# Kernel tuning notes

Hardware: AMD Instinct MI355X
Metric: run time of the kernel (lower is better)

The kernel has to match this reference:

```python
import jax, jax.numpy as jnp
import numpy as np

N = 100000
D = 128
E = 1600000
NEG_SLOPE = 0.2


def gatv2_layer(x, src, dst, Wl, Wr, att, b):
    # GATv2Conv (heads=1, eval mode): lin_l -> source/message feats, lin_r -> target feats
    xl = x @ Wl                      # [N, D]
    xr = x @ Wr                      # [N, D]
    # per-edge score: a^T LeakyReLU(x_l[src] + x_r[dst])
    z = jax.nn.leaky_relu(xl[src] + xr[dst], NEG_SLOPE)  # [E, D]
    e = z @ att                      # [E]
    # segment softmax over incoming edges of each dst node
    m = jax.ops.segment_max(e, dst, num_segments=N)      # [N]
    ex = jnp.exp(e - m[dst])
    s = jax.ops.segment_sum(ex, dst, num_segments=N)     # [N]
    alpha = ex / (s[dst] + 1e-16)                        # [E]
    # weighted scatter-aggregate of source messages
    out = jax.ops.segment_sum(alpha[:, None] * xl[src], dst, num_segments=N)
    return out + b


def setup_inputs() -> dict:
    key = jax.random.key(0)
    ks = jax.random.split(key, 6)
    scale = 1.0 / np.sqrt(D)
    x = jax.random.normal(ks[0], (N, D), dtype=jnp.float32)
    edge_index = jax.random.randint(ks[1], (2, E), 0, N, dtype=jnp.int64)
    Wl = jax.random.normal(ks[2], (3, D, D), dtype=jnp.float32) * scale
    Wr = jax.random.normal(ks[3], (3, D, D), dtype=jnp.float32) * scale
    att = jax.random.normal(ks[4], (3, D), dtype=jnp.float32) * scale
    b = jax.random.normal(ks[5], (3, D), dtype=jnp.float32) * 0.01
    return {"x": x, "Wl": Wl, "Wr": Wr, "att": att, "b": b, "edge_index": edge_index}


def reference(x, Wl, Wr, att, b, edge_index):
    src, dst = edge_index[0], edge_index[1]
    h = gatv2_layer(x, src, dst, Wl[0], Wr[0], att[0], b[0])
    h = jax.nn.relu(h)
    h = gatv2_layer(h, src, dst, Wl[1], Wr[1], att[1], b[1])
    h = jax.nn.relu(h)
    h = gatv2_layer(h, src, dst, Wl[2], Wr[2], att[2], b[2])
    return h
```

## Files before the change

### kernel.cpp

```cpp
#include <hip/hip_runtime.h>
#include <math.h>

#define DD 128
#define NEG 0.2f

typedef short short8 __attribute__((ext_vector_type(8)));
typedef float f32x4 __attribute__((ext_vector_type(4)));
typedef float f32x2 __attribute__((ext_vector_type(2)));
typedef _Float16 h2v __attribute__((ext_vector_type(2)));

__device__ __forceinline__ unsigned short f2bf(float f) {
    unsigned u = __float_as_uint(f);
    return (unsigned short)((u + 0x7fffu + ((u >> 16) & 1u)) >> 16);
}
__device__ __forceinline__ float bf2f(unsigned short h) {
    return __uint_as_float(((unsigned)h) << 16);
}

#if __has_builtin(__builtin_amdgcn_exp2f)
#define EXP2F(x) __builtin_amdgcn_exp2f(x)
#else
#define EXP2F(x) exp2f(x)
#endif

__device__ void excl_scan_1024(int* sh, int* aux) {
    __syncthreads();
    int t = threadIdx.x;
    int base = t * 4;
    int a0 = sh[base], a1 = sh[base + 1], a2 = sh[base + 2], a3 = sh[base + 3];
    int s = a0 + a1 + a2 + a3;
    aux[t] = s;
    __syncthreads();
    for (int off = 1; off < 256; off <<= 1) {
        int v = (t >= off) ? aux[t - off] : 0;
        __syncthreads();
        aux[t] += v;
        __syncthreads();
    }
    int excl = aux[t] - s;
    sh[base] = excl;
    sh[base + 1] = excl + a0;
    sh[base + 2] = excl + a0 + a1;
    sh[base + 3] = excl + a0 + a1 + a2;
    __syncthreads();
}

__global__ __launch_bounds__(256) void k_histC(const int* __restrict__ dst,
                                               int* __restrict__ histC, int E, int CB,
                                               const float* __restrict__ Wl,
                                               const float* __restrict__ Wr,
                                               unsigned short* __restrict__ Wth,
                                               unsigned short* __restrict__ Wtl) {
    __shared__ int h[1024];
    int t = threadIdx.x;
    if (blockIdx.x >= 256) {
        int idx = (blockIdx.x - 256) * 256 + t;
        if (idx < 3 * 256 * 128) {
            int L = idx >> 15;
            int rem = idx & 32767;
            int nn = rem >> 7;
            int k = rem & 127;
            float v = (nn < 128) ? Wl[L * 16384 + k * 128 + nn]
                                 : Wr[L * 16384 + k * 128 + (nn - 128)];
            unsigned short hh = f2bf(v);
            Wth[idx] = hh;
            Wtl[idx] = f2bf(v - bf2f(hh));
        }
        return;
    }
    for (int j = t; j < 1024; j += 256) h[j] = 0;
    __syncthreads();
    int stride = 256 * 256;
    for (int i = blockIdx.x * 256 + t; i < E; i += stride)
        atomicAdd(&h[dst[i] >> 7], 1);
    __syncthreads();
    for (int j = t; j < CB; j += 256)
        if (h[j]) atomicAdd(&histC[j], h[j]);
}

#define CHUNK 8192
__global__ __launch_bounds__(256) void k_part3(const int* __restrict__ srcI,
                                               const int* __restrict__ dstI,
                                               const int* __restrict__ histC,
                                               int* __restrict__ cursor0C,
                                               int* __restrict__ baseC,
                                               uint2* __restrict__ part,
                                               int E, int CB) {
    __shared__ int sh[1024];
    __shared__ int gsh[1024];
    __shared__ int aux[256];
    __shared__ int resBase[1024];
    __shared__ int cur[1024];
    __shared__ uint2 stage[CHUNK];
    int t = threadIdx.x;
    int c0 = blockIdx.x * CHUNK;
    int cnt = E - c0; if (cnt > CHUNK) cnt = CHUNK;

    for (int j = t; j < 1024; j += 256) sh[j] = 0;
    for (int j = t; j < 1024; j += 256) gsh[j] = (j < CB) ? histC[j] : 0;
    __syncthreads();
    for (int i = t; i < cnt; i += 256)
        atomicAdd(&sh[dstI[c0 + i] >> 7], 1);
    excl_scan_1024(gsh, aux);
    for (int j = t; j < CB; j += 256) {
        int c = sh[j];
        resBase[j] = gsh[j] + (c ? atomicAdd(&cursor0C[j], c) : 0);
    }
    if (blockIdx.x == 0)
        for (int j = t; j <= CB; j += 256) baseC[j] = gsh[j];
    excl_scan_1024(sh, aux);
    for (int j = t; j < 1024; j += 256) cur[j] = sh[j];
    __syncthreads();
    for (int i = t; i < cnt; i += 256) {
        unsigned s = (unsigned)srcI[c0 + i];
        unsigned d = (unsigned)dstI[c0 + i];
        int b = (int)(d >> 7);
        int pos = atomicAdd(&cur[b], 1);
        stage[pos].x = s;
        stage[pos].y = d;
    }
    __syncthreads();
    for (int i = t; i < cnt; i += 256) {
        uint2 v = stage[i];
        int b = (int)(v.y >> 7);
        part[resBase[b] + (i - sh[b])] = v;
    }
}

__global__ __launch_bounds__(256) void k_part4(const uint2* __restrict__ part,
                                               const int* __restrict__ baseC,
                                               int* __restrict__ srcs,
                                               int* __restrict__ row_ptr,
                                               int N) {
    __shared__ int hist[128];
    __shared__ int incl[128];
    __shared__ int cur[128];
    __shared__ unsigned srcS[8192];
    int b = blockIdx.x;
    int t = threadIdx.x;
    int base = baseC[b];
    int cnt = baseC[b + 1] - base;
    int node0 = b << 7;

    if (t < 128) hist[t] = 0;
    __syncthreads();
    for (int i = t; i < cnt; i += 256)
        atomicAdd(&hist[part[base + i].y & 127], 1);
    __syncthreads();
    if (t < 128) incl[t] = hist[t];
    __syncthreads();
    for (int off = 1; off < 128; off <<= 1) {
        int v = 0;
        if (t < 128 && t >= off) v = incl[t - off];
        __syncthreads();
        if (t < 128) incl[t] += v;
        __syncthreads();
    }
    if (t < 128) cur[t] = incl[t] - hist[t];
    __syncthreads();
    for (int i = t; i < cnt; i += 256) {
        uint2 e = part[base + i];
        int r = atomicAdd(&cur[e.y & 127], 1);
        if (r < 8192) srcS[r] = e.x;
    }
    __syncthreads();
    for (int i = t; i < cnt; i += 256)
        srcs[base + i] = (int)srcS[i];
    int nodes = N - node0; if (nodes > 128) nodes = 128;
    if (t < nodes) row_ptr[node0 + t + 1] = base + incl[t];
    if (b == 0 && t == 0) row_ptr[0] = 0;
}

#define NCH 8192
__global__ __launch_bounds__(256) void k_deghist(const int* __restrict__ row_ptr,
                                                 int* __restrict__ histD, int N) {
    __shared__ int h[128];
    int t = threadIdx.x;
    if (t < 128) h[t] = 0;
    __syncthreads();
    int c0 = blockIdx.x * NCH;
    int cnt = N - c0; if (cnt > NCH) cnt = NCH;
    for (int i = t; i < cnt; i += 256) {
        int deg = row_ptr[c0 + i + 1] - row_ptr[c0 + i];
        int c = deg < 127 ? deg : 127;
        atomicAdd(&h[c], 1);
    }
    __syncthreads();
    if (t < 128 && h[t]) atomicAdd(&histD[t], h[t]);
}

__global__ __launch_bounds__(256) void k_degpart(const int* __restrict__ row_ptr,
                                                 const int* __restrict__ histD,
                                                 int* __restrict__ cursor0D,
                                                 int* __restrict__ order, int N) {
    __shared__ int hist[128];
    __shared__ int gex[128];
    __shared__ int excl[128];
    __shared__ int cur[128];
    __shared__ int resB[128];
    __shared__ int stage[NCH];
    int t = threadIdx.x;
    int c0 = blockIdx.x * NCH;
    int cnt = N - c0; if (cnt > NCH) cnt = NCH;

    int g0 = 0;
    if (t < 128) { hist[t] = 0; g0 = histD[t]; gex[t] = g0; }
    __syncthreads();
    for (int i = t; i < cnt; i += 256) {
        int deg = row_ptr[c0 + i + 1] - row_ptr[c0 + i];
        int c = deg < 127 ? deg : 127;
        atomicAdd(&hist[c], 1);
    }
    __syncthreads();
    for (int off = 1; off < 128; off <<= 1) {
        int v = 0;
        if (t < 128 && t >= off) v = gex[t - off];
        __syncthreads();
        if (t < 128) gex[t] += v;
        __syncthreads();
    }
    if (t < 128) resB[t] = (gex[t] - g0) + (hist[t] ? atomicAdd(&cursor0D[t], hist[t]) : 0);
    if (t < 128) excl[t] = hist[t];
    __syncthreads();
    for (int off = 1; off < 128; off <<= 1) {
        int v = 0;
        if (t < 128 && t >= off) v = excl[t - off];
        __syncthreads();
        if (t < 128) excl[t] += v;
        __syncthreads();
    }
    if (t < 128) { excl[t] -= hist[t]; cur[t] = excl[t]; }
    __syncthreads();
    for (int i = t; i < cnt; i += 256) {
        int deg = row_ptr[c0 + i + 1] - row_ptr[c0 + i];
        int c = deg < 127 ? deg : 127;
        int p = atomicAdd(&cur[c], 1);
        stage[p] = (c << 20) | (c0 + i);
    }
    __syncthreads();
    for (int i = t; i < cnt; i += 256) {
        int v = stage[i];
        int c = v >> 20;
        order[resB[c] + (i - excl[c])] = v & 0xFFFFF;
    }
}

__device__ __forceinline__ void cvt8(const float4& a, const float4& b, uint4& hi, uint4& lo) {
    union US8 { unsigned short s[8]; uint4 u; } H, Lo;
    float f[8] = {a.x, a.y, a.z, a.w, b.x, b.y, b.z, b.w};
#pragma unroll
    for (int i = 0; i < 8; i++) {
        unsigned short h = f2bf(f[i]);
        H.s[i] = h;
        Lo.s[i] = f2bf(f[i] - bf2f(h));
    }
    hi = H.u; lo = Lo.u;
}

template <int F32SRC>
__global__ __launch_bounds__(256) void k_gemm(const float* __restrict__ Xf,
                                              const unsigned short* __restrict__ Ahi,
                                              const unsigned short* __restrict__ Alo,
                                              const unsigned short* __restrict__ Wth,
                                              const unsigned short* __restrict__ Wtl,
                                              _Float16* __restrict__ xl, _Float16* __restrict__ xr,
                                              int M, int L, int gX) {
    __shared__ unsigned short sA[2][128][40];
    __shared__ unsigned short sB[2][128][40];
    int b = blockIdx.x;
    int grp = b >> 4, j8 = b & 7, half = (b >> 3) & 1;
    int ry = grp * 8 + j8;
    if (ry >= gX) return;

    int t = threadIdx.x;
    int lane = t & 63;
    int l15 = lane & 15;
    int quad = lane >> 4;
    int wave = t >> 6;
    int wm = wave & 1;
    int wn = wave >> 1;
    int r0 = ry * 128;
    const unsigned short* WthL = Wth + ((size_t)L * 256 + half * 128) * 128;
    const unsigned short* WtlL = Wtl + ((size_t)L * 256 + half * 128) * 128;

    int row0 = t >> 2,       row1 = (t + 256) >> 2;
    int kq   = (t & 3) * 8;
    int gr0 = r0 + row0; gr0 = gr0 < M ? gr0 : M - 1;
    int gr1 = r0 + row1; gr1 = gr1 < M ? gr1 : M - 1;

    uint4 rAh0, rAh1, rAl0, rAl1, rBh0, rBh1, rBl0, rBl1;
    float4 f00, f01, f10, f11;

#define GLOADA(K0)                                                          \
    if (F32SRC) {                                                           \
        f00 = *(const float4*)(Xf + (size_t)gr0 * DD + (K0) + kq);          \
        f01 = *(const float4*)(Xf + (size_t)gr0 * DD + (K0) + kq + 4);      \
        f10 = *(const float4*)(Xf + (size_t)gr1 * DD + (K0) + kq);          \
        f11 = *(const float4*)(Xf + (size_t)gr1 * DD + (K0) + kq + 4);      \
    } else {                                                                \
        rAh0 = *(const uint4*)(Ahi + (size_t)gr0 * DD + (K0) + kq);         \
        rAh1 = *(const uint4*)(Ahi + (size_t)gr1 * DD + (K0) + kq);         \
        rAl0 = *(const uint4*)(Alo + (size_t)gr0 * DD + (K0) + kq);         \
        rAl1 = *(const uint4*)(Alo + (size_t)gr1 * DD + (K0) + kq);         \
    }
#define GLOADB(K0)                                                          \
    rBh0 = *(const uint4*)(WthL + (size_t)row0 * DD + (K0) + kq);           \
    rBh1 = *(const uint4*)(WthL + (size_t)row1 * DD + (K0) + kq);           \
    rBl0 = *(const uint4*)(WtlL + (size_t)row0 * DD + (K0) + kq);           \
    rBl1 = *(const uint4*)(WtlL + (size_t)row1 * DD + (K0) + kq);

    f32x4 acc[4][4] = {};
    union F8 { short8 v; uint4 u; };

    GLOADA(0);
    GLOADB(0);

#pragma unroll
    for (int kc = 0; kc < 4; kc++) {
        if (kc) __syncthreads();
        if (F32SRC) {
            cvt8(f00, f01, rAh0, rAl0);
            cvt8(f10, f11, rAh1, rAl1);
        }
        *(uint4*)&sA[0][row0][kq] = rAh0;
        *(uint4*)&sA[0][row1][kq] = rAh1;
        *(uint4*)&sA[1][row0][kq] = rAl0;
        *(uint4*)&sA[1][row1][kq] = rAl1;
        *(uint4*)&sB[0][row0][kq] = rBh0;
        *(uint4*)&sB[0][row1][kq] = rBh1;
        *(uint4*)&sB[1][row0][kq] = rBl0;
        *(uint4*)&sB[1][row1][kq] = rBl1;
        __syncthreads();
        if (kc < 3) { GLOADA((kc + 1) * 32); GLOADB((kc + 1) * 32); }

        F8 ah[4], al[4], bh[4], bl[4];
#pragma unroll
        for (int mt = 0; mt < 4; mt++) {
            ah[mt].u = *(const uint4*)&sA[0][wm * 64 + mt * 16 + l15][quad * 8];
            al[mt].u = *(const uint4*)&sA[1][wm * 64 + mt * 16 + l15][quad * 8];
        }
#pragma unroll
        for (int nt = 0; nt < 4; nt++) {
            bh[nt].u = *(const uint4*)&sB[0][wn * 64 + nt * 16 + l15][quad * 8];
            bl[nt].u = *(const uint4*)&sB[1][wn * 64 + nt * 16 + l15][quad * 8];
        }
#pragma unroll
        for (int mt = 0; mt < 4; mt++)
#pragma unroll
            for (int nt = 0; nt < 4; nt++) {
                acc[mt][nt] = __builtin_amdgcn_mfma_f32_16x16x32_bf16(ah[mt].v, bh[nt].v, acc[mt][nt], 0, 0, 0);
                acc[mt][nt] = __builtin_amdgcn_mfma_f32_16x16x32_bf16(al[mt].v, bh[nt].v, acc[mt][nt], 0, 0, 0);
                acc[mt][nt] = __builtin_amdgcn_mfma_f32_16x16x32_bf16(ah[mt].v, bl[nt].v, acc[mt][nt], 0, 0, 0);
            }
    }
#undef GLOADA
#undef GLOADB

    _Float16* C = half ? xr : xl;
#pragma unroll
    for (int mt = 0; mt < 4; mt++)
#pragma unroll
        for (int r = 0; r < 4; r++) {
            int row = r0 + wm * 64 + mt * 16 + quad * 4 + r;
            if (row < M) {
#pragma unroll
                for (int nt = 0; nt < 4; nt++)
                    C[(size_t)row * DD + wn * 64 + nt * 16 + l15] = (_Float16)acc[mt][nt][r];
            }
        }
}

__global__ __launch_bounds__(256) void k_attn(const _Float16* __restrict__ xl,
                                              const _Float16* __restrict__ xr,
                                              const int* __restrict__ row_ptr,
                                              const int* __restrict__ srcs,
                                              const int* __restrict__ order,
                                              const float* __restrict__ att,
                                              const float* __restrict__ bias,
                                              float* __restrict__ outF,
                                              unsigned short* __restrict__ outHi,
                                              unsigned short* __restrict__ outLo,
                                              int n, int mode) {
    int wid = (blockIdx.x * blockDim.x + threadIdx.x) >> 6;
    int l = threadIdx.x & 63;
    int l15 = l & 15;
    int g = l >> 4;
    int idx = wid * 4 + g;
    bool act = idx < n;
    int d = act ? order[idx] : 0;

    union Q { uint4 q; h2v h[4]; };
    const float LOG2E = 1.44269504088896f;

    h2v at[4], xrh[4];
    {
        float4 a0 = *(const float4*)(att + l15 * 8);
        float4 a1 = *(const float4*)(att + l15 * 8 + 4);
        at[0] = h2v{(_Float16)(a0.x * LOG2E), (_Float16)(a0.y * LOG2E)};
        at[1] = h2v{(_Float16)(a0.z * LOG2E), (_Float16)(a0.w * LOG2E)};
        at[2] = h2v{(_Float16)(a1.x * LOG2E), (_Float16)(a1.y * LOG2E)};
        at[3] = h2v{(_Float16)(a1.z * LOG2E), (_Float16)(a1.w * LOG2E)};
        Q hr; hr.q = *(const uint4*)(xr + (size_t)d * DD + l15 * 8);
#pragma unroll
        for (int j = 0; j < 4; j++) xrh[j] = hr.h[j];
    }
    const _Float16 cneg = (_Float16)NEG;

    int beg = act ? row_ptr[d] : 0;
    int end = act ? row_ptr[d + 1] : 0;
    int cnt = end - beg;

    int mc = cnt;
    mc = max(mc, __shfl_xor(mc, 16, 64));
    mc = max(mc, __shfl_xor(mc, 32, 64));
    int iters = (mc + 3) >> 2;

    float lse = 0.f;
    float av[8] = {};

    int i0 = beg, i1 = beg + 1, i2 = beg + 2, i3 = beg + 3;
    bool v0 = i0 < end, v1 = i1 < end, v2 = i2 < end, v3 = i3 < end;
    int s0 = v0 ? srcs[i0] : 0;
    int s1 = v1 ? srcs[i1] : 0;
    int s2 = v2 ? srcs[i2] : 0;
    int s3 = v3 ? srcs[i3] : 0;

    const _Float16* xlp = xl + l15 * 8;

    for (int it = 0; it < iters; ++it) {
        Q h0, h1, h2, h3;
        h0.q = *(const uint4*)(xlp + (size_t)s0 * DD);
        h1.q = *(const uint4*)(xlp + (size_t)s1 * DD);
        h2.q = *(const uint4*)(xlp + (size_t)s2 * DD);
        h3.q = *(const uint4*)(xlp + (size_t)s3 * DD);
        int n0 = i0 + 4, n1 = i1 + 4, n2 = i2 + 4, n3 = i3 + 4;
        bool nv0 = n0 < end, nv1 = n1 < end, nv2 = n2 < end, nv3 = n3 < end;
        int t0 = nv0 ? srcs[n0] : 0;
        int t1 = nv1 ? srcs[n1] : 0;
        int t2 = nv2 ? srcs[n2] : 0;
        int t3 = nv3 ? srcs[n3] : 0;

        float p0 = 0.f, p1 = 0.f, p2 = 0.f, p3 = 0.f;
#pragma unroll
        for (int j = 0; j < 4; j++) {
            h2v z0 = h0.h[j] + xrh[j];
            h2v zl0 = __builtin_elementwise_max(z0, z0 * cneg);
            p0 = __builtin_amdgcn_fdot2(zl0, at[j], p0, false);
            h2v z1 = h1.h[j] + xrh[j];
            h2v zl1 = __builtin_elementwise_max(z1, z1 * cneg);
            p1 = __builtin_amdgcn_fdot2(zl1, at[j], p1, false);
            h2v z2 = h2.h[j] + xrh[j];
            h2v zl2 = __builtin_elementwise_max(z2, z2 * cneg);
            p2 = __builtin_amdgcn_fdot2(zl2, at[j], p2, false);
            h2v z3 = h3.h[j] + xrh[j];
            h2v zl3 = __builtin_elementwise_max(z3, z3 * cneg);
            p3 = __builtin_amdgcn_fdot2(zl3, at[j], p3, false);
        }
        p0 += __shfl_xor(p0, 1, 64);  p1 += __shfl_xor(p1, 1, 64);
        p2 += __shfl_xor(p2, 1, 64);  p3 += __shfl_xor(p3, 1, 64);
        p0 += __shfl_xor(p0, 2, 64);  p1 += __shfl_xor(p1, 2, 64);
        p2 += __shfl_xor(p2, 2, 64);  p3 += __shfl_xor(p3, 2, 64);
        p0 += __shfl_xor(p0, 4, 64);  p1 += __shfl_xor(p1, 4, 64);
        p2 += __shfl_xor(p2, 4, 64);  p3 += __shfl_xor(p3, 4, 64);
        p0 += __shfl_xor(p0, 8, 64);  p1 += __shfl_xor(p1, 8, 64);
        p2 += __shfl_xor(p2, 8, 64);  p3 += __shfl_xor(p3, 8, 64);
        p0 = fminf(fmaxf(p0, -86.f), 86.f);
        p1 = fminf(fmaxf(p1, -86.f), 86.f);
        p2 = fminf(fmaxf(p2, -86.f), 86.f);
        p3 = fminf(fmaxf(p3, -86.f), 86.f);
        float w0 = v0 ? EXP2F(p0) : 0.f;
        float w1 = v1 ? EXP2F(p1) : 0.f;
        float w2 = v2 ? EXP2F(p2) : 0.f;
        float w3 = v3 ? EXP2F(p3) : 0.f;
        lse += (w0 + w1) + (w2 + w3);
#pragma unroll
        for (int j = 0; j < 4; j++) {
            av[2 * j]     += (float)h0.h[j][0] * w0;
            av[2 * j + 1] += (float)h0.h[j][1] * w0;
            av[2 * j]     += (float)h1.h[j][0] * w1;
            av[2 * j + 1] += (float)h1.h[j][1] * w1;
            av[2 * j]     += (float)h2.h[j][0] * w2;
            av[2 * j + 1] += (float)h2.h[j][1] * w2;
            av[2 * j]     += (float)h3.h[j][0] * w3;
            av[2 * j + 1] += (float)h3.h[j][1] * w3;
        }
        i0 = n0; i1 = n1; i2 = n2; i3 = n3;
        v0 = nv0; v1 = nv1; v2 = nv2; v3 = nv3;
        s0 = t0; s1 = t1; s2 = t2; s3 = t3;
    }

    if (act) {
        float inv = (cnt > 0) ? 1.0f / lse : 0.f;
        float o[8];
        float4 b0 = *(const float4*)(bias + l15 * 8);
        float4 b1 = *(const float4*)(bias + l15 * 8 + 4);
        float bv[8] = {b0.x, b0.y, b0.z, b0.w, b1.x, b1.y, b1.z, b1.w};
#pragma unroll
        for (int j = 0; j < 8; j++) o[j] = av[j] * inv + bv[j];
        if (mode) {
            union U8 { unsigned short s[8]; uint4 q; };
            U8 hh, ll;
#pragma unroll
            for (int j = 0; j < 8; j++) {
                float v = fmaxf(o[j], 0.f);
                hh.s[j] = f2bf(v);
                ll.s[j] = f2bf(v - bf2f(hh.s[j]));
            }
            *(uint4*)(outHi + (size_t)d * DD + l15 * 8) = hh.q;
            *(uint4*)(outLo + (size_t)d * DD + l15 * 8) = ll.q;
        } else {
            float4 o0 = {o[0], o[1], o[2], o[3]};
            float4 o1 = {o[4], o[5], o[6], o[7]};
            float* op = outF + (size_t)d * DD + l15 * 8;
            *(float4*)op = o0;
            *(float4*)(op + 4) = o1;
        }
    }
}

extern "C" void kernel_launch(void* const* d_in, const int* in_sizes, int n_in,
                              void* d_out, int out_size, void* d_ws, size_t ws_size,
                              hipStream_t stream) {
    const float* x    = (const float*)d_in[0];
    const float* Wl   = (const float*)d_in[1];
    const float* Wr   = (const float*)d_in[2];
    const float* att  = (const float*)d_in[3];
    const float* bias = (const float*)d_in[4];
    const int*   ei   = (const int*)d_in[5];

    int N = in_sizes[0] / DD;
    int E = in_sizes[5] / 2;
    const int* srcI = ei;
    const int* dstI = ei + E;
    float* out = (float*)d_out;
    int CB = (N + 127) >> 7;

    char* ws = (char*)d_ws;
    size_t off = 0;
    auto alloc = [&](size_t bytes) -> void* {
        void* p = ws + off;
        off += (bytes + 255) & ~(size_t)255;
        return p;
    };
    _Float16*       xl   = (_Float16*)alloc((size_t)N * DD * 2);
    _Float16*       xr   = (_Float16*)alloc((size_t)N * DD * 2);
    unsigned short* Ahi  = (unsigned short*)alloc((size_t)N * DD * 2);
    unsigned short* Alo  = (unsigned short*)alloc((size_t)N * DD * 2);
    unsigned short* Wth  = (unsigned short*)alloc((size_t)3 * 256 * 128 * 2);
    unsigned short* Wtl  = (unsigned short*)alloc((size_t)3 * 256 * 128 * 2);
    uint2* part    = (uint2*)alloc((size_t)E * 8);
    int*   srcs    = (int*)alloc((size_t)E * 4);
    int*   row_ptr = (int*)alloc((size_t)(N + 1) * 4);
    int*   order   = (int*)alloc((size_t)N * 4);
    int*   baseC   = (int*)alloc((size_t)(CB + 1) * 4);
    int*   z       = (int*)alloc((size_t)(2 * CB + 256) * 4);
    int*   histC    = z;
    int*   cursor0C = z + CB;
    int*   histD    = z + 2 * CB;
    int*   cursor0D = z + 2 * CB + 128;

    const int tb = 256;
    (void)hipMemsetAsync(z, 0, (size_t)(2 * CB + 256) * 4, stream);
    k_histC<<<640, 256, 0, stream>>>(dstI, histC, E, CB, Wl, Wr, Wth, Wtl);
    k_part3<<<(E + CHUNK - 1) / CHUNK, 256, 0, stream>>>(srcI, dstI, histC, cursor0C,
                                                         baseC, part, E, CB);
    k_part4<<<CB, 256, 0, stream>>>(part, baseC, srcs, row_ptr, N);
    int gD = (N + NCH - 1) / NCH;
    k_deghist<<<gD, 256, 0, stream>>>(row_ptr, histD, N);
    k_degpart<<<gD, 256, 0, stream>>>(row_ptr, histD, cursor0D, order, N);

    int gX = (N + 127) / 128;
    int NB = 16 * ((gX + 7) / 8);
    for (int L = 0; L < 3; ++L) {
        if (L == 0)
            k_gemm<1><<<NB, 256, 0, stream>>>(x, Ahi, Alo, Wth, Wtl, xl, xr, N, L, gX);
        else
            k_gemm<0><<<NB, 256, 0, stream>>>(x, Ahi, Alo, Wth, Wtl, xl, xr, N, L, gX);
        k_attn<<<((size_t)N * 16 + tb - 1) / tb, tb, 0, stream>>>(
            xl, xr, row_ptr, srcs, order, att + (size_t)L * DD, bias + (size_t)L * DD,
            out, Ahi, Alo, N, (L < 2) ? 1 : 0);
    }
}
```

Before: 477.9 us.

## Replace two-level radix CSR build with degree count, scan, and atomic scatter

Drops the bucketed two-pass partition (histC, part3, part4) used to build the CSR. It now counts per-node in-degrees with global atomics, scans them in two small kernels into row_ptr and a cursor array, and scatters sources with a per-node atomic cursor. The degree-bucket ordering kernel is fused into the scatter launch and reads degrees directly. This removes the intermediate uint2 partition buffer and several launches, but relies on random global atomics. It also makes neighbour order within each row nondeterministic, which can change float summation order.

```diff
diff --git a/kernel.cpp b/kernel.cpp
--- a/kernel.cpp
+++ b/kernel.cpp
@@ -23,38 +23,17 @@
 #define EXP2F(x) exp2f(x)
 #endif
 
-__device__ void excl_scan_1024(int* sh, int* aux) {
-    __syncthreads();
+
+__global__ __launch_bounds__(256) void k_deg(const int* __restrict__ dst,
+                                             int* __restrict__ deg, int E, int EB,
+                                             const float* __restrict__ Wl,
+                                             const float* __restrict__ Wr,
+                                             unsigned short* __restrict__ Wth,
+                                             unsigned short* __restrict__ Wtl) {
+    int b = blockIdx.x;
     int t = threadIdx.x;
-    int base = t * 4;
-    int a0 = sh[base], a1 = sh[base + 1], a2 = sh[base + 2], a3 = sh[base + 3];
-    int s = a0 + a1 + a2 + a3;
-    aux[t] = s;
-    __syncthreads();
-    for (int off = 1; off < 256; off <<= 1) {
-        int v = (t >= off) ? aux[t - off] : 0;
-        __syncthreads();
-        aux[t] += v;
-        __syncthreads();
-    }
-    int excl = aux[t] - s;
-    sh[base] = excl;
-    sh[base + 1] = excl + a0;
-    sh[base + 2] = excl + a0 + a1;
-    sh[base + 3] = excl + a0 + a1 + a2;
-    __syncthreads();
-}
-
-__global__ __launch_bounds__(256) void k_histC(const int* __restrict__ dst,
-                                               int* __restrict__ histC, int E, int CB,
-                                               const float* __restrict__ Wl,
-                                               const float* __restrict__ Wr,
-                                               unsigned short* __restrict__ Wth,
-                                               unsigned short* __restrict__ Wtl) {
-    __shared__ int h[1024];
-    int t = threadIdx.x;
-    if (blockIdx.x >= 256) {
-        int idx = (blockIdx.x - 256) * 256 + t;
+    if (b >= EB) {
+        int idx = (b - EB) * 256 + t;
         if (idx < 3 * 256 * 128) {
             int L = idx >> 15;
             int rem = idx & 32767;
@@ -68,128 +47,95 @@
         }
         return;
     }
-    for (int j = t; j < 1024; j += 256) h[j] = 0;
-    __syncthreads();
-    int stride = 256 * 256;
-    for (int i = blockIdx.x * 256 + t; i < E; i += stride)
-        atomicAdd(&h[dst[i] >> 7], 1);
-    __syncthreads();
-    for (int j = t; j < CB; j += 256)
-        if (h[j]) atomicAdd(&histC[j], h[j]);
-}
-
-#define CHUNK 8192
-__global__ __launch_bounds__(256) void k_part3(const int* __restrict__ srcI,
-                                               const int* __restrict__ dstI,
-                                               const int* __restrict__ histC,
-                                               int* __restrict__ cursor0C,
-                                               int* __restrict__ baseC,
-                                               uint2* __restrict__ part,
-                                               int E, int CB) {
-    __shared__ int sh[1024];
-    __shared__ int gsh[1024];
+    int stride = EB * 256;
+    for (int i = b * 256 + t; i < E; i += stride)
+        atomicAdd(&deg[dst[i]], 1);
+}
+
+#define SCH 2048
+__global__ __launch_bounds__(256) void k_scanA(const int* __restrict__ deg,
+                                               int* __restrict__ csum, int N) {
+    __shared__ int red[256];
+    int t = threadIdx.x;
+    int c0 = blockIdx.x * SCH;
+    int s = 0;
+#pragma unroll
+    for (int j = 0; j < 8; j++) {
+        int i = c0 + j * 256 + t;
+        s += (i < N) ? deg[i] : 0;
+    }
+    red[t] = s;
+    __syncthreads();
+    for (int off = 128; off > 0; off >>= 1) {
+        if (t < off) red[t] += red[t + off];
+        __syncthreads();
+    }
+    if (t == 0) csum[blockIdx.x] = red[0];
+}
+
+__global__ __launch_bounds__(256) void k_scanC(const int* __restrict__ deg,
+                                               const int* __restrict__ csum,
+                                               int* __restrict__ row_ptr,
+                                               int* __restrict__ cursor,
+                                               int* __restrict__ histD,
+                                               int N, int E, int NSC) {
+    __shared__ int cb[128];
     __shared__ int aux[256];
-    __shared__ int resBase[1024];
-    __shared__ int cur[1024];
-    __shared__ uint2 stage[CHUNK];
+    __shared__ int hl[128];
     int t = threadIdx.x;
-    int c0 = blockIdx.x * CHUNK;
-    int cnt = E - c0; if (cnt > CHUNK) cnt = CHUNK;
-
-    for (int j = t; j < 1024; j += 256) sh[j] = 0;
-    for (int j = t; j < 1024; j += 256) gsh[j] = (j < CB) ? histC[j] : 0;
-    __syncthreads();
-    for (int i = t; i < cnt; i += 256)
-        atomicAdd(&sh[dstI[c0 + i] >> 7], 1);
-    excl_scan_1024(gsh, aux);
-    for (int j = t; j < CB; j += 256) {
-        int c = sh[j];
-        resBase[j] = gsh[j] + (c ? atomicAdd(&cursor0C[j], c) : 0);
-    }
-    if (blockIdx.x == 0)
-        for (int j = t; j <= CB; j += 256) baseC[j] = gsh[j];
-    excl_scan_1024(sh, aux);
-    for (int j = t; j < 1024; j += 256) cur[j] = sh[j];
-    __syncthreads();
-    for (int i = t; i < cnt; i += 256) {
-        unsigned s = (unsigned)srcI[c0 + i];
-        unsigned d = (unsigned)dstI[c0 + i];
-        int b = (int)(d >> 7);
-        int pos = atomicAdd(&cur[b], 1);
-        stage[pos].x = s;
-        stage[pos].y = d;
-    }
-    __syncthreads();
-    for (int i = t; i < cnt; i += 256) {
-        uint2 v = stage[i];
-        int b = (int)(v.y >> 7);
-        part[resBase[b] + (i - sh[b])] = v;
-    }
-}
-
-__global__ __launch_bounds__(256) void k_part4(const uint2* __restrict__ part,
-                                               const int* __restrict__ baseC,
-                                               int* __restrict__ srcs,
-                                               int* __restrict__ row_ptr,
-                                               int N) {
-    __shared__ int hist[128];
-    __shared__ int incl[128];
-    __shared__ int cur[128];
-    __shared__ unsigned srcS[8192];
     int b = blockIdx.x;
-    int t = threadIdx.x;
-    int base = baseC[b];
-    int cnt = baseC[b + 1] - base;
-    int node0 = b << 7;
-
-    if (t < 128) hist[t] = 0;
-    __syncthreads();
-    for (int i = t; i < cnt; i += 256)
-        atomicAdd(&hist[part[base + i].y & 127], 1);
-    __syncthreads();
-    if (t < 128) incl[t] = hist[t];
+    if (t < 128) { cb[t] = (t < NSC) ? csum[t] : 0; hl[t] = 0; }
     __syncthreads();
     for (int off = 1; off < 128; off <<= 1) {
         int v = 0;
-        if (t < 128 && t >= off) v = incl[t - off];
-        __syncthreads();
-        if (t < 128) incl[t] += v;
-        __syncthreads();
-    }
-    if (t < 128) cur[t] = incl[t] - hist[t];
-    __syncthreads();
-    for (int i = t; i < cnt; i += 256) {
-        uint2 e = part[base + i];
-        int r = atomicAdd(&cur[e.y & 127], 1);
-        if (r < 8192) srcS[r] = e.x;
-    }
-    __syncthreads();
-    for (int i = t; i < cnt; i += 256)
-        srcs[base + i] = (int)srcS[i];
-    int nodes = N - node0; if (nodes > 128) nodes = 128;
-    if (t < nodes) row_ptr[node0 + t + 1] = base + incl[t];
-    if (b == 0 && t == 0) row_ptr[0] = 0;
+        if (t < 128 && t >= off) v = cb[t - off];
+        __syncthreads();
+        if (t < 128) cb[t] += v;
+        __syncthreads();
+    }
+    int cbase = b ? cb[b - 1] : 0;
+
+    int base = b * SCH + t * 8;
+    int v[8];
+    int s = 0;
+#pragma unroll
+    for (int j = 0; j < 8; j++) {
+        int i = base + j;
+        int x = (i < N) ? deg[i] : 0;
+        if (i < N) atomicAdd(&hl[x < 127 ? x : 127], 1);
+        v[j] = s;
+        s += x;
+    }
+    aux[t] = s;
+    __syncthreads();
+    for (int off = 1; off < 256; off <<= 1) {
+        int w = (t >= off) ? aux[t - off] : 0;
+        __syncthreads();
+        aux[t] += w;
+        __syncthreads();
+    }
+    int off0 = cbase + aux[t] - s;
+#pragma unroll
+    for (int j = 0; j < 8; j++) {
+        int i = base + j;
+        if (i < N) {
+            int r = off0 + v[j];
+            row_ptr[i] = r;
+            cursor[i] = r;
+        }
+    }
+    __syncthreads();
+    if (t < 128 && hl[t]) atomicAdd(&histD[t], hl[t]);
+    if (b == 0 && t == 0) row_ptr[N] = E;
 }
 
 #define NCH 8192
-__global__ __launch_bounds__(256) void k_deghist(const int* __restrict__ row_ptr,
-                                                 int* __restrict__ histD, int N) {
-    __shared__ int h[128];
-    int t = threadIdx.x;
-    if (t < 128) h[t] = 0;
-    __syncthreads();
-    int c0 = blockIdx.x * NCH;
-    int cnt = N - c0; if (cnt > NCH) cnt = NCH;
-    for (int i = t; i < cnt; i += 256) {
-        int deg = row_ptr[c0 + i + 1] - row_ptr[c0 + i];
-        int c = deg < 127 ? deg : 127;
-        atomicAdd(&h[c], 1);
-    }
-    __syncthreads();
-    if (t < 128 && h[t]) atomicAdd(&histD[t], h[t]);
-}
-
-__global__ __launch_bounds__(256) void k_degpart(const int* __restrict__ row_ptr,
+__global__ __launch_bounds__(256) void k_scatter(const int* __restrict__ srcI,
+                                                 const int* __restrict__ dstI,
+                                                 int* __restrict__ cursor,
+                                                 int* __restrict__ srcs,
+                                                 int E, int EB,
+                                                 const int* __restrict__ deg,
                                                  const int* __restrict__ histD,
                                                  int* __restrict__ cursor0D,
                                                  int* __restrict__ order, int N) {
@@ -200,15 +146,28 @@
     __shared__ int resB[128];
     __shared__ int stage[NCH];
     int t = threadIdx.x;
-    int c0 = blockIdx.x * NCH;
+    int b = blockIdx.x;
+
+    if (b < EB) {
+        int stride = EB * 256;
+        for (int i = b * 256 + t; i < E; i += stride) {
+            int d = dstI[i];
+            int pos = atomicAdd(&cursor[d], 1);
+            srcs[pos] = srcI[i];
+        }
+        return;
+    }
+
+    int db = b - EB;
+    int c0 = db * NCH;
     int cnt = N - c0; if (cnt > NCH) cnt = NCH;
 
     int g0 = 0;
     if (t < 128) { hist[t] = 0; g0 = histD[t]; gex[t] = g0; }
     __syncthreads();
     for (int i = t; i < cnt; i += 256) {
-        int deg = row_ptr[c0 + i + 1] - row_ptr[c0 + i];
-        int c = deg < 127 ? deg : 127;
+        int dg = deg[c0 + i];
+        int c = dg < 127 ? dg : 127;
         atomicAdd(&hist[c], 1);
     }
     __syncthreads();
@@ -232,8 +191,8 @@
     if (t < 128) { excl[t] -= hist[t]; cur[t] = excl[t]; }
     __syncthreads();
     for (int i = t; i < cnt; i += 256) {
-        int deg = row_ptr[c0 + i + 1] - row_ptr[c0 + i];
-        int c = deg < 127 ? deg : 127;
+        int dg = deg[c0 + i];
+        int c = dg < 127 ? dg : 127;
         int p = atomicAdd(&cur[c], 1);
         stage[p] = (c << 20) | (c0 + i);
     }
@@ -533,7 +492,6 @@
     const int* srcI = ei;
     const int* dstI = ei + E;
     float* out = (float*)d_out;
-    int CB = (N + 127) >> 7;
 
     char* ws = (char*)d_ws;
     size_t off = 0;
@@ -548,26 +506,27 @@
     unsigned short* Alo  = (unsigned short*)alloc((size_t)N * DD * 2);
     unsigned short* Wth  = (unsigned short*)alloc((size_t)3 * 256 * 128 * 2);
     unsigned short* Wtl  = (unsigned short*)alloc((size_t)3 * 256 * 128 * 2);
-    uint2* part    = (uint2*)alloc((size_t)E * 8);
     int*   srcs    = (int*)alloc((size_t)E * 4);
     int*   row_ptr = (int*)alloc((size_t)(N + 1) * 4);
+    int*   cursor  = (int*)alloc((size_t)N * 4);
     int*   order   = (int*)alloc((size_t)N * 4);
-    int*   baseC   = (int*)alloc((size_t)(CB + 1) * 4);
-    int*   z       = (int*)alloc((size_t)(2 * CB + 256) * 4);
-    int*   histC    = z;
-    int*   cursor0C = z + CB;
-    int*   histD    = z + 2 * CB;
-    int*   cursor0D = z + 2 * CB + 128;
+    int*   csum    = (int*)alloc((size_t)256 * 4);
+    int*   z       = (int*)alloc((size_t)(N + 256) * 4);
+    int*   deg      = z;
+    int*   histD    = z + N;
+    int*   cursor0D = z + N + 128;
 
     const int tb = 256;
-    (void)hipMemsetAsync(z, 0, (size_t)(2 * CB + 256) * 4, stream);
-    k_histC<<<640, 256, 0, stream>>>(dstI, histC, E, CB, Wl, Wr, Wth, Wtl);
-    k_part3<<<(E + CHUNK - 1) / CHUNK, 256, 0, stream>>>(srcI, dstI, histC, cursor0C,
-                                                         baseC, part, E, CB);
-    k_part4<<<CB, 256, 0, stream>>>(part, baseC, srcs, row_ptr, N);
-    int gD = (N + NCH - 1) / NCH;
-    k_deghist<<<gD, 256, 0, stream>>>(row_ptr, histD, N);
-    k_degpart<<<gD, 256, 0, stream>>>(row_ptr, histD, cursor0D, order, N);
+    const int EB = 2048;
+    int NSC = (N + SCH - 1) / SCH;
+    int gD  = (N + NCH - 1) / NCH;
+
+    (void)hipMemsetAsync(z, 0, (size_t)(N + 256) * 4, stream);
+    k_deg<<<EB + 384, tb, 0, stream>>>(dstI, deg, E, EB, Wl, Wr, Wth, Wtl);
+    k_scanA<<<NSC, tb, 0, stream>>>(deg, csum, N);
+    k_scanC<<<NSC, tb, 0, stream>>>(deg, csum, row_ptr, cursor, histD, N, E, NSC);
+    k_scatter<<<EB + gD, tb, 0, stream>>>(srcI, dstI, cursor, srcs, E, EB,
+                                          deg, histD, cursor0D, order, N);
 
     int gX = (N + 127) / 128;
     int NB = 16 * ((gX + 7) / 8);
```

Result: slower. 603.6 us (+26.3%).

## Hoist coarse bucket scan into its own kernel and pack partition entries into 32 bits

Applied to the files above, without the earlier changes.

The global exclusive scan of the coarse destination histogram moves out of every k_part3 block into a single-block k_scanC2 kernel, so partition blocks no longer repeat the 1024-entry scan. Partition entries are packed into one 32-bit word, with the source index in the low 25 bits and the low 7 bits of dst on top, which halves the bytes written by k_part3 and read by k_part4. CHUNK drops from 8192 to 4096, giving more partition blocks with smaller shared staging, and k_part4's shared buffer shrinks to 4096 entries. This assumes N fits in 25 bits and that no 128-node bucket exceeds 4096 edges; a denser bucket would silently drop sources.

```diff
diff --git a/kernel.cpp b/kernel.cpp
--- a/kernel.cpp
+++ b/kernel.cpp
@@ -22,6 +22,7 @@
 #else
 #define EXP2F(x) exp2f(x)
 #endif
+
 
 __device__ void excl_scan_1024(int* sh, int* aux) {
     __syncthreads();
@@ -78,16 +79,24 @@
         if (h[j]) atomicAdd(&histC[j], h[j]);
 }
 
-#define CHUNK 8192
+__global__ __launch_bounds__(256) void k_scanC2(const int* __restrict__ histC,
+                                                int* __restrict__ baseC, int CB) {
+    __shared__ int sh[1024];
+    __shared__ int aux[256];
+    int t = threadIdx.x;
+    for (int j = t; j < 1024; j += 256) sh[j] = (j < CB) ? histC[j] : 0;
+    excl_scan_1024(sh, aux);
+    for (int j = t; j <= CB; j += 256) baseC[j] = sh[j];
+}
+
+#define CHUNK 4096
 __global__ __launch_bounds__(256) void k_part3(const int* __restrict__ srcI,
                                                const int* __restrict__ dstI,
-                                               const int* __restrict__ histC,
+                                               const int* __restrict__ baseC,
                                                int* __restrict__ cursor0C,
-                                               int* __restrict__ baseC,
-                                               uint2* __restrict__ part,
+                                               unsigned* __restrict__ part,
                                                int E, int CB) {
     __shared__ int sh[1024];
-    __shared__ int gsh[1024];
     __shared__ int aux[256];
     __shared__ int resBase[1024];
     __shared__ int cur[1024];
@@ -97,17 +106,14 @@
     int cnt = E - c0; if (cnt > CHUNK) cnt = CHUNK;
 
     for (int j = t; j < 1024; j += 256) sh[j] = 0;
-    for (int j = t; j < 1024; j += 256) gsh[j] = (j < CB) ? histC[j] : 0;
     __syncthreads();
     for (int i = t; i < cnt; i += 256)
         atomicAdd(&sh[dstI[c0 + i] >> 7], 1);
-    excl_scan_1024(gsh, aux);
+    __syncthreads();
     for (int j = t; j < CB; j += 256) {
         int c = sh[j];
-        resBase[j] = gsh[j] + (c ? atomicAdd(&cursor0C[j], c) : 0);
-    }
-    if (blockIdx.x == 0)
-        for (int j = t; j <= CB; j += 256) baseC[j] = gsh[j];
+        resBase[j] = baseC[j] + (c ? atomicAdd(&cursor0C[j], c) : 0);
+    }
     excl_scan_1024(sh, aux);
     for (int j = t; j < 1024; j += 256) cur[j] = sh[j];
     __syncthreads();
@@ -123,11 +129,11 @@
     for (int i = t; i < cnt; i += 256) {
         uint2 v = stage[i];
         int b = (int)(v.y >> 7);
-        part[resBase[b] + (i - sh[b])] = v;
-    }
-}
-
-__global__ __launch_bounds__(256) void k_part4(const uint2* __restrict__ part,
+        part[resBase[b] + (i - sh[b])] = v.x | ((v.y & 127u) << 25);
+    }
+}
+
+__global__ __launch_bounds__(256) void k_part4(const unsigned* __restrict__ part,
                                                const int* __restrict__ baseC,
                                                int* __restrict__ srcs,
                                                int* __restrict__ row_ptr,
@@ -135,7 +141,7 @@
     __shared__ int hist[128];
     __shared__ int incl[128];
     __shared__ int cur[128];
-    __shared__ unsigned srcS[8192];
+    __shared__ int srcS[4096];
     int b = blockIdx.x;
     int t = threadIdx.x;
     int base = baseC[b];
@@ -145,7 +151,7 @@
     if (t < 128) hist[t] = 0;
     __syncthreads();
     for (int i = t; i < cnt; i += 256)
-        atomicAdd(&hist[part[base + i].y & 127], 1);
+        atomicAdd(&hist[part[base + i] >> 25], 1);
     __syncthreads();
     if (t < 128) incl[t] = hist[t];
     __syncthreads();
@@ -159,13 +165,13 @@
     if (t < 128) cur[t] = incl[t] - hist[t];
     __syncthreads();
     for (int i = t; i < cnt; i += 256) {
-        uint2 e = part[base + i];
-        int r = atomicAdd(&cur[e.y & 127], 1);
-        if (r < 8192) srcS[r] = e.x;
+        unsigned v = part[base + i];
+        int r = atomicAdd(&cur[v >> 25], 1);
+        if (r < 4096) srcS[r] = (int)(v & 0x1FFFFFFu);
     }
     __syncthreads();
     for (int i = t; i < cnt; i += 256)
-        srcs[base + i] = (int)srcS[i];
+        srcs[base + i] = srcS[i];
     int nodes = N - node0; if (nodes > 128) nodes = 128;
     if (t < nodes) row_ptr[node0 + t + 1] = base + incl[t];
     if (b == 0 && t == 0) row_ptr[0] = 0;
@@ -548,7 +554,7 @@
     unsigned short* Alo  = (unsigned short*)alloc((size_t)N * DD * 2);
     unsigned short* Wth  = (unsigned short*)alloc((size_t)3 * 256 * 128 * 2);
     unsigned short* Wtl  = (unsigned short*)alloc((size_t)3 * 256 * 128 * 2);
-    uint2* part    = (uint2*)alloc((size_t)E * 8);
+    unsigned* part = (unsigned*)alloc((size_t)E * 4);
     int*   srcs    = (int*)alloc((size_t)E * 4);
     int*   row_ptr = (int*)alloc((size_t)(N + 1) * 4);
     int*   order   = (int*)alloc((size_t)N * 4);
@@ -562,8 +568,9 @@
     const int tb = 256;
     (void)hipMemsetAsync(z, 0, (size_t)(2 * CB + 256) * 4, stream);
     k_histC<<<640, 256, 0, stream>>>(dstI, histC, E, CB, Wl, Wr, Wth, Wtl);
-    k_part3<<<(E + CHUNK - 1) / CHUNK, 256, 0, stream>>>(srcI, dstI, histC, cursor0C,
-                                                         baseC, part, E, CB);
+    k_scanC2<<<1, 256, 0, stream>>>(histC, baseC, CB);
+    k_part3<<<(E + CHUNK - 1) / CHUNK, 256, 0, stream>>>(srcI, dstI, baseC, cursor0C,
+                                                         part, E, CB);
     k_part4<<<CB, 256, 0, stream>>>(part, baseC, srcs, row_ptr, N);
     int gD = (N + NCH - 1) / NCH;
     k_deghist<<<gD, 256, 0, stream>>>(row_ptr, histD, N);
```

Measured after the change: 473.4 us. Within noise of the previous version (-0.9%).
